# Optimization experiments

Measured on AMD Instinct MI355X. Metric: run time of the kernel, lower is better.

## Reference

```python
import jax, jax.numpy as jnp
import numpy as np

THRESH_SCALE = 0.05

def ste_ternary(w):
    # forward: quantize to {-1,0,+1}; backward: straight-through (identity)
    thr = THRESH_SCALE * jnp.mean(jnp.abs(w))
    q = jnp.where(w > thr, 1.0, jnp.where(w < -thr, -1.0, 0.0)).astype(w.dtype)
    return w + jax.lax.stop_gradient(q - w)

def setup_inputs() -> dict:
    key = jax.random.key(0)
    kx, kw = jax.random.split(key)
    x = jax.random.normal(kx, (8192, 4096), dtype=jnp.float32)
    weight = jax.random.normal(kw, (4096, 4096), dtype=jnp.float32) * 0.1
    return {"x": x, "weight": weight}

def reference(x, weight):
    w_t = ste_ternary(weight)          # [out, in] in {-1,0,+1}
    return x @ w_t.T                    # [tokens, out]
```

## Files before the change

kernel.cpp:

```cpp
#include <hip/hip_runtime.h>
#include <hip/hip_bf16.h>
#include <stdint.h>


typedef __attribute__((ext_vector_type(4))) int i32x4;

#define KDIM 4096
#define NDIM 4096

#define M_ROWS 8192
#define ABS_BLOCKS 1024

__device__ inline void gld_lds16(const void* g, void* l) {
  __builtin_amdgcn_global_load_lds(
      (__attribute__((address_space(1))) void*)g,
      (__attribute__((address_space(3))) void*)l,
      16, 0, 0);
}

__device__ inline int pack4(int a, int b, int c, int d) {
  return (a & 255) | ((b & 255) << 8) | ((c & 255) << 16) | (d << 24);
}

__device__ inline int q8(float v, float inv) {
  int q = __float2int_rn(v * inv);
  return q > 127 ? 127 : (q < -127 ? -127 : q);
}

__global__ __launch_bounds__(256) void prep_kernel(
    const float4* __restrict__ x, signed char* __restrict__ xq,
    float* __restrict__ steps, const float4* __restrict__ w, int wn4,
    double* __restrict__ sum) {
  if (blockIdx.x < M_ROWS) {
    const int row = blockIdx.x;
    const float4* xr = x + (size_t)row * 1024;
    float4 v[4];
    float amax = 0.0f;
#pragma unroll
    for (int j = 0; j < 4; ++j) {
      v[j] = xr[threadIdx.x + 256 * j];
      amax = fmaxf(amax, fmaxf(fmaxf(fabsf(v[j].x), fabsf(v[j].y)),
                               fmaxf(fabsf(v[j].z), fabsf(v[j].w))));
    }
#pragma unroll
    for (int off = 32; off > 0; off >>= 1)
      amax = fmaxf(amax, __shfl_down(amax, off, 64));
    __shared__ float wmax[4];
    const int lane = threadIdx.x & 63, wave = threadIdx.x >> 6;
    if (lane == 0) wmax[wave] = amax;
    __syncthreads();
    const float m = fmaxf(fmaxf(wmax[0], wmax[1]), fmaxf(wmax[2], wmax[3]));
    const float inv = m > 0.0f ? 127.0f / m : 0.0f;
    if (threadIdx.x == 0) steps[row] = m > 0.0f ? m / 127.0f : 0.0f;
    int* out = (int*)(xq + (size_t)row * 4096);
#pragma unroll
    for (int j = 0; j < 4; ++j) {
      out[threadIdx.x + 256 * j] = pack4(q8(v[j].x, inv), q8(v[j].y, inv),
                                         q8(v[j].z, inv), q8(v[j].w, inv));
    }
  } else {
    double s = 0.0;
    const int stride = ABS_BLOCKS * 256;
    for (int i = (blockIdx.x - M_ROWS) * 256 + threadIdx.x; i < wn4;
         i += stride) {
      float4 v = w[i];
      s += (double)((fabsf(v.x) + fabsf(v.y)) + (fabsf(v.z) + fabsf(v.w)));
    }
#pragma unroll
    for (int off = 32; off > 0; off >>= 1) s += __shfl_down(s, off, 64);
    __shared__ double wsum[4];
    const int lane = threadIdx.x & 63, wave = threadIdx.x >> 6;
    if (lane == 0) wsum[wave] = s;
    __syncthreads();
    if (threadIdx.x == 0) atomicAdd(sum, wsum[0] + wsum[1] + wsum[2] + wsum[3]);
  }
}

__global__ __launch_bounds__(256) void quant_kernel(
    const float4* __restrict__ w, const double* __restrict__ sum,
    int* __restrict__ q, int n4, double inv_n) {
  const float thr = (float)(0.05 * (*sum) * inv_n);
  const int stride = gridDim.x * blockDim.x;
  for (int i = blockIdx.x * blockDim.x + threadIdx.x; i < n4; i += stride) {
    float4 v = w[i];
    int a = v.x > thr ? 1 : (v.x < -thr ? -1 : 0);
    int b = v.y > thr ? 1 : (v.y < -thr ? -1 : 0);
    int c = v.z > thr ? 1 : (v.z < -thr ? -1 : 0);
    int d = v.w > thr ? 1 : (v.w < -thr ? -1 : 0);
    q[i] = pack4(a, b, c, d);
  }
}

#define MFMA_I8 __builtin_amdgcn_mfma_i32_16x16x64_i8

__global__ __launch_bounds__(512, 2) void gemm_i8_1b(
    const signed char* __restrict__ A, const signed char* __restrict__ B,
    const float* __restrict__ steps, float* __restrict__ C, int M) {
  __shared__ unsigned char lds[131072];

  const int tid = threadIdx.x;
  const int lane = tid & 63;
  const int w = tid >> 6;

  const int bm = blockIdx.y * 256;
  const int bn = blockIdx.x * 256;

  const int rL = lane >> 3;
  const int csw = (((lane & 7) ^ rL) << 4);
  const signed char* aBase = A + (size_t)(bm + w * 8 + rL) * KDIM + csw;
  const signed char* bBase = B + (size_t)(bn + w * 8 + rL) * KDIM + csw;
  unsigned char* const ldsA = lds;
  unsigned char* const ldsB = lds + 65536;

  const int fr = lane & 15;
  const int fk = (lane >> 4) * 16;
  const int xr = (lane & 7) << 4;
  const int cc0 = fk ^ xr;
  const int cc1 = (64 + fk) ^ xr;
  const int wm = (w >> 2) * 128;
  const int wn = (w & 3) * 64;
  const int aro = (wm + fr) * 128;
  const int bro = (wn + fr) * 128;

  i32x4 acc[8][4] = {};

  gld_lds16(bBase, ldsB + w * 1024);
  gld_lds16(bBase + (size_t)64 * KDIM, ldsB + 8192 + w * 1024);
  gld_lds16(bBase + (size_t)128 * KDIM, ldsB + 16384 + w * 1024);
  gld_lds16(bBase + (size_t)192 * KDIM, ldsB + 16384 + 8192 + w * 1024);
  gld_lds16(aBase, ldsA + w * 1024);
  gld_lds16(aBase + (size_t)64 * KDIM, ldsA + 8192 + w * 1024);
  gld_lds16(aBase + (size_t)128 * KDIM, ldsA + 16384 + w * 1024);
  gld_lds16(aBase + (size_t)192 * KDIM, ldsA + 16384 + 8192 + w * 1024);
  asm volatile("s_waitcnt vmcnt(0)" ::: "memory");
  __builtin_amdgcn_s_barrier();
  __builtin_amdgcn_sched_barrier(0);

  for (int t = 0; t < 32; ++t) {
    const int b = t & 1;
    const unsigned char* Ab = ldsA + b * 32768;
    const unsigned char* Bb = ldsB + b * 32768;

    i32x4 bfr[4][2], af0[8], af1[8];
#pragma unroll
    for (int ni = 0; ni < 4; ++ni) {
      bfr[ni][0] = *(const i32x4*)(Bb + bro + ni * 2048 + cc0);
      bfr[ni][1] = *(const i32x4*)(Bb + bro + ni * 2048 + cc1);
    }
#pragma unroll
    for (int m = 0; m < 8; ++m)
      af0[m] = *(const i32x4*)(Ab + aro + m * 2048 + cc0);

    if (t + 1 < 32) {
      unsigned char* An = ldsA + (b ^ 1) * 32768;
      unsigned char* Bn = ldsB + (b ^ 1) * 32768;
      const signed char* aS = aBase + (size_t)(t + 1) * 128;
      const signed char* bS = bBase + (size_t)(t + 1) * 128;
      gld_lds16(bS, Bn + w * 1024);
      gld_lds16(bS + (size_t)64 * KDIM, Bn + 8192 + w * 1024);
      gld_lds16(bS + (size_t)128 * KDIM, Bn + 16384 + w * 1024);
      gld_lds16(bS + (size_t)192 * KDIM, Bn + 16384 + 8192 + w * 1024);
      gld_lds16(aS, An + w * 1024);
      gld_lds16(aS + (size_t)64 * KDIM, An + 8192 + w * 1024);
      gld_lds16(aS + (size_t)128 * KDIM, An + 16384 + w * 1024);
      gld_lds16(aS + (size_t)192 * KDIM, An + 16384 + 8192 + w * 1024);
    }

    __builtin_amdgcn_s_setprio(1);
#pragma unroll
    for (int m = 0; m < 4; ++m)
#pragma unroll
      for (int ni = 0; ni < 4; ++ni)
        acc[m][ni] = MFMA_I8(af0[m], bfr[ni][0], acc[m][ni], 0, 0, 0);
    __builtin_amdgcn_s_setprio(0);

#pragma unroll
    for (int m = 0; m < 8; ++m)
      af1[m] = *(const i32x4*)(Ab + aro + m * 2048 + cc1);

    __builtin_amdgcn_s_setprio(1);
#pragma unroll
    for (int m = 4; m < 8; ++m)
#pragma unroll
      for (int ni = 0; ni < 4; ++ni)
        acc[m][ni] = MFMA_I8(af0[m], bfr[ni][0], acc[m][ni], 0, 0, 0);
#pragma unroll
    for (int m = 0; m < 8; ++m)
#pragma unroll
      for (int ni = 0; ni < 4; ++ni)
        acc[m][ni] = MFMA_I8(af1[m], bfr[ni][1], acc[m][ni], 0, 0, 0);
    __builtin_amdgcn_s_setprio(0);

    if (t + 1 < 32) {
      asm volatile("s_waitcnt vmcnt(0)" ::: "memory");
      __builtin_amdgcn_s_barrier();
      __builtin_amdgcn_sched_barrier(0);
    }
  }

  const int cn = lane & 15;
  const int cm = (lane >> 4) * 4;
  float stp[8][4];
#pragma unroll
  for (int mi = 0; mi < 8; ++mi)
#pragma unroll
    for (int r = 0; r < 4; ++r)
      stp[mi][r] = steps[bm + wm + mi * 16 + cm + r];
#pragma unroll
  for (int mi = 0; mi < 8; ++mi) {
#pragma unroll
    for (int ni = 0; ni < 4; ++ni) {
#pragma unroll
      for (int r = 0; r < 4; ++r) {
        const int m = bm + wm + mi * 16 + cm + r;
        const int n = bn + wn + ni * 16 + cn;
        C[(size_t)m * NDIM + n] = (float)acc[mi][ni][r] * stp[mi][r];
      }
    }
  }
}

extern "C" void kernel_launch(void* const* d_in, const int* in_sizes, int n_in,
                              void* d_out, int out_size, void* d_ws,
                              size_t ws_size, hipStream_t stream) {
  const float* x = (const float*)d_in[0];
  const float* w = (const float*)d_in[1];
  float* out = (float*)d_out;

  const int K = 4096;
  const int N = 4096;
  const int M = in_sizes[0] / K;
  const int NW = in_sizes[1];

  char* ws = (char*)d_ws;
  double* d_sum = (double*)ws;
  float* steps = (float*)(ws + 256);
  signed char* qb = (signed char*)(ws + 65536);
  signed char* xq = qb + (size_t)N * K;

  hipMemsetAsync(d_sum, 0, sizeof(double), stream);
  prep_kernel<<<M_ROWS + ABS_BLOCKS, 256, 0, stream>>>(
      (const float4*)x, xq, steps, (const float4*)w, NW / 4, d_sum);
  quant_kernel<<<2048, 256, 0, stream>>>((const float4*)w, d_sum, (int*)qb,
                                         NW / 4, 1.0 / NW);
  dim3 grid(N / 256, M / 256);
  gemm_i8_1b<<<grid, 512, 0, stream>>>(xq, qb, steps, out, M);
}
```

Measured before the change: 387.2 us.

## Load pre-swizzled ternary weights directly to registers and triple-buffer A in LDS

The quantize kernel now writes the ternary weight matrix in an MFMA-fragment-friendly tiled layout. The GEMM then loads B fragments straight from global memory into registers instead of staging them through LDS. The freed LDS holds a three-stage ring buffer for A, with prefetch two steps ahead and partial vmcnt waits. This removes LDS traffic and bank pressure for B, but B loads now go through registers each iteration and rely on L2 reuse across blocks. It also hardcodes M_ROWS for the grid.

New measurement: 395.7 us. +2.2%, slower.

```diff
diff --git a/kernel.cpp b/kernel.cpp
--- a/kernel.cpp
+++ b/kernel.cpp
@@ -78,7 +78,7 @@
 
 __global__ __launch_bounds__(256) void quant_kernel(
     const float4* __restrict__ w, const double* __restrict__ sum,
-    int* __restrict__ q, int n4, double inv_n) {
+    signed char* __restrict__ qt, int n4, double inv_n) {
   const float thr = (float)(0.05 * (*sum) * inv_n);
   const int stride = gridDim.x * blockDim.x;
   for (int i = blockIdx.x * blockDim.x + threadIdx.x; i < n4; i += stride) {
@@ -87,16 +87,19 @@
     int b = v.y > thr ? 1 : (v.y < -thr ? -1 : 0);
     int c = v.z > thr ? 1 : (v.z < -thr ? -1 : 0);
     int d = v.w > thr ? 1 : (v.w < -thr ? -1 : 0);
-    q[i] = pack4(a, b, c, d);
+    const int n = i >> 10;
+    const int k0 = (i & 1023) * 4;
+    *(int*)(qt + (size_t)(n >> 4) * 65536 + (k0 >> 4) * 256 + (n & 15) * 16 +
+            (k0 & 15)) = pack4(a, b, c, d);
   }
 }
 
 #define MFMA_I8 __builtin_amdgcn_mfma_i32_16x16x64_i8
 
-__global__ __launch_bounds__(512, 2) void gemm_i8_1b(
-    const signed char* __restrict__ A, const signed char* __restrict__ B,
-    const float* __restrict__ steps, float* __restrict__ C, int M) {
-  __shared__ unsigned char lds[131072];
+__global__ __launch_bounds__(512, 2) void gemm_i8_bd(
+    const signed char* __restrict__ A, const signed char* __restrict__ qbT,
+    const float* __restrict__ steps, float* __restrict__ C) {
+  __shared__ unsigned char ldsA[98304];
 
   const int tid = threadIdx.x;
   const int lane = tid & 63;
@@ -108,9 +111,7 @@
   const int rL = lane >> 3;
   const int csw = (((lane & 7) ^ rL) << 4);
   const signed char* aBase = A + (size_t)(bm + w * 8 + rL) * KDIM + csw;
-  const signed char* bBase = B + (size_t)(bn + w * 8 + rL) * KDIM + csw;
-  unsigned char* const ldsA = lds;
-  unsigned char* const ldsB = lds + 65536;
+  const int sb = w * 1024;
 
   const int fr = lane & 15;
   const int fk = (lane >> 4) * 16;
@@ -120,59 +121,56 @@
   const int wm = (w >> 2) * 128;
   const int wn = (w & 3) * 64;
   const int aro = (wm + fr) * 128;
-  const int bro = (wn + fr) * 128;
+
+  const signed char* qbW = qbT + (size_t)((bn + wn) >> 4) * 65536 + lane * 16;
 
   i32x4 acc[8][4] = {};
-
-  gld_lds16(bBase, ldsB + w * 1024);
-  gld_lds16(bBase + (size_t)64 * KDIM, ldsB + 8192 + w * 1024);
-  gld_lds16(bBase + (size_t)128 * KDIM, ldsB + 16384 + w * 1024);
-  gld_lds16(bBase + (size_t)192 * KDIM, ldsB + 16384 + 8192 + w * 1024);
-  gld_lds16(aBase, ldsA + w * 1024);
-  gld_lds16(aBase + (size_t)64 * KDIM, ldsA + 8192 + w * 1024);
-  gld_lds16(aBase + (size_t)128 * KDIM, ldsA + 16384 + w * 1024);
-  gld_lds16(aBase + (size_t)192 * KDIM, ldsA + 16384 + 8192 + w * 1024);
-  asm volatile("s_waitcnt vmcnt(0)" ::: "memory");
-  __builtin_amdgcn_s_barrier();
-  __builtin_amdgcn_sched_barrier(0);
-
+  i32x4 bf[4][2];
+
+  {
+    gld_lds16(aBase, ldsA + sb);
+    gld_lds16(aBase + (size_t)64 * KDIM, ldsA + 8192 + sb);
+    gld_lds16(aBase + (size_t)128 * KDIM, ldsA + 16384 + sb);
+    gld_lds16(aBase + (size_t)192 * KDIM, ldsA + 24576 + sb);
+    const signed char* a1 = aBase + 128;
+    gld_lds16(a1, ldsA + 32768 + sb);
+    gld_lds16(a1 + (size_t)64 * KDIM, ldsA + 32768 + 8192 + sb);
+    gld_lds16(a1 + (size_t)128 * KDIM, ldsA + 32768 + 16384 + sb);
+    gld_lds16(a1 + (size_t)192 * KDIM, ldsA + 32768 + 24576 + sb);
+#pragma unroll
+    for (int ni = 0; ni < 4; ++ni)
+#pragma unroll
+      for (int kk = 0; kk < 2; ++kk)
+        bf[ni][kk] = *(const i32x4*)(qbW + ni * 65536 + kk * 1024);
+    asm volatile("s_waitcnt vmcnt(12)" ::: "memory");
+    __builtin_amdgcn_s_barrier();
+    __builtin_amdgcn_sched_barrier(0);
+  }
+
+#pragma unroll 1
   for (int t = 0; t < 32; ++t) {
-    const int b = t & 1;
-    const unsigned char* Ab = ldsA + b * 32768;
-    const unsigned char* Bb = ldsB + b * 32768;
-
-    i32x4 bfr[4][2], af0[8], af1[8];
-#pragma unroll
-    for (int ni = 0; ni < 4; ++ni) {
-      bfr[ni][0] = *(const i32x4*)(Bb + bro + ni * 2048 + cc0);
-      bfr[ni][1] = *(const i32x4*)(Bb + bro + ni * 2048 + cc1);
-    }
+    const unsigned char* Ab = (const unsigned char*)ldsA + (t % 3) * 32768;
+    i32x4 af0[8], af1[8];
 #pragma unroll
     for (int m = 0; m < 8; ++m)
       af0[m] = *(const i32x4*)(Ab + aro + m * 2048 + cc0);
 
-    if (t + 1 < 32) {
-      unsigned char* An = ldsA + (b ^ 1) * 32768;
-      unsigned char* Bn = ldsB + (b ^ 1) * 32768;
-      const signed char* aS = aBase + (size_t)(t + 1) * 128;
-      const signed char* bS = bBase + (size_t)(t + 1) * 128;
-      gld_lds16(bS, Bn + w * 1024);
-      gld_lds16(bS + (size_t)64 * KDIM, Bn + 8192 + w * 1024);
-      gld_lds16(bS + (size_t)128 * KDIM, Bn + 16384 + w * 1024);
-      gld_lds16(bS + (size_t)192 * KDIM, Bn + 16384 + 8192 + w * 1024);
-      gld_lds16(aS, An + w * 1024);
-      gld_lds16(aS + (size_t)64 * KDIM, An + 8192 + w * 1024);
-      gld_lds16(aS + (size_t)128 * KDIM, An + 16384 + w * 1024);
-      gld_lds16(aS + (size_t)192 * KDIM, An + 16384 + 8192 + w * 1024);
-    }
-
     __builtin_amdgcn_s_setprio(1);
 #pragma unroll
     for (int m = 0; m < 4; ++m)
 #pragma unroll
       for (int ni = 0; ni < 4; ++ni)
-        acc[m][ni] = MFMA_I8(af0[m], bfr[ni][0], acc[m][ni], 0, 0, 0);
+        acc[m][ni] = MFMA_I8(af0[m], bf[ni][0], acc[m][ni], 0, 0, 0);
     __builtin_amdgcn_s_setprio(0);
+
+    if (t + 2 < 32) {
+      unsigned char* An = (unsigned char*)ldsA + ((t + 2) % 3) * 32768;
+      const signed char* aS = aBase + (size_t)(t + 2) * 128;
+      gld_lds16(aS, An + sb);
+      gld_lds16(aS + (size_t)64 * KDIM, An + 8192 + sb);
+      gld_lds16(aS + (size_t)128 * KDIM, An + 16384 + sb);
+      gld_lds16(aS + (size_t)192 * KDIM, An + 24576 + sb);
+    }
 
 #pragma unroll
     for (int m = 0; m < 8; ++m)
@@ -183,16 +181,22 @@
     for (int m = 4; m < 8; ++m)
 #pragma unroll
       for (int ni = 0; ni < 4; ++ni)
-        acc[m][ni] = MFMA_I8(af0[m], bfr[ni][0], acc[m][ni], 0, 0, 0);
+        acc[m][ni] = MFMA_I8(af0[m], bf[ni][0], acc[m][ni], 0, 0, 0);
 #pragma unroll
     for (int m = 0; m < 8; ++m)
 #pragma unroll
       for (int ni = 0; ni < 4; ++ni)
-        acc[m][ni] = MFMA_I8(af1[m], bfr[ni][1], acc[m][ni], 0, 0, 0);
+        acc[m][ni] = MFMA_I8(af1[m], bf[ni][1], acc[m][ni], 0, 0, 0);
     __builtin_amdgcn_s_setprio(0);
 
     if (t + 1 < 32) {
-      asm volatile("s_waitcnt vmcnt(0)" ::: "memory");
+#pragma unroll
+      for (int ni = 0; ni < 4; ++ni)
+#pragma unroll
+        for (int kk = 0; kk < 2; ++kk)
+          bf[ni][kk] = *(const i32x4*)(qbW + ni * 65536 + (t + 1) * 2048 +
+                                       kk * 1024);
+      asm volatile("s_waitcnt vmcnt(8)" ::: "memory");
       __builtin_amdgcn_s_barrier();
       __builtin_amdgcn_sched_barrier(0);
     }
@@ -229,7 +233,6 @@
 
   const int K = 4096;
   const int N = 4096;
-  const int M = in_sizes[0] / K;
   const int NW = in_sizes[1];
 
   char* ws = (char*)d_ws;
@@ -241,8 +244,8 @@
   hipMemsetAsync(d_sum, 0, sizeof(double), stream);
   prep_kernel<<<M_ROWS + ABS_BLOCKS, 256, 0, stream>>>(
       (const float4*)x, xq, steps, (const float4*)w, NW / 4, d_sum);
-  quant_kernel<<<2048, 256, 0, stream>>>((const float4*)w, d_sum, (int*)qb,
-                                         NW / 4, 1.0 / NW);
-  dim3 grid(N / 256, M / 256);
-  gemm_i8_1b<<<grid, 512, 0, stream>>>(xq, qb, steps, out, M);
-}
+  quant_kernel<<<2048, 256, 0, stream>>>((const float4*)w, d_sum, qb, NW / 4,
+                                         1.0 / NW);
+  dim3 grid(N / 256, M_ROWS / 256);
+  gemm_i8_bd<<<grid, 512, 0, stream>>>(xq, qb, steps, out);
+}
```
